# Kernel tuning notes

Hardware: AMD Instinct MI355X
Metric: run time of the kernel (lower is better)

## Reference

```python
import jax, jax.numpy as jnp
import numpy as np

B, L, C = 512, 2048, 32  # batch, seq_len, num_labels


def setup_inputs() -> dict:
    key = jax.random.key(0)
    k1, k2, k3 = jax.random.split(key, 3)
    emissions = jax.random.normal(k1, (B, L, C), dtype=jnp.float32)
    tags = jax.random.randint(k2, (B, L), 0, C, dtype=jnp.int32)
    mask = jnp.ones((B, L), dtype=jnp.int32)
    # learned parameter: transitions (num_labels, num_labels)
    transitions = jax.random.normal(k3, (C, C), dtype=jnp.float32)
    return {"emissions": emissions, "transitions": transitions, "tags": tags, "mask": mask}


def _crf_nll(emissions, transitions, tags, mask):
    Bn, Ln, Cn = emissions.shape
    maskf = mask.astype(emissions.dtype)

    # ---- gold-path score (vectorized over the t loop) ----
    # emit[b,t] = emissions[b,t,tags[b,t]] for t in [0, L-2]
    emit = jnp.take_along_axis(emissions[:, : Ln - 1], tags[:, : Ln - 1, None], axis=2)[..., 0]
    # trans[b,t] = transitions[tags[b,t], tags[b,t+1]]
    trans = transitions[tags[:, : Ln - 1], tags[:, 1:]]
    score = jnp.sum(emit * maskf[:, : Ln - 1] + trans * maskf[:, 1:], axis=1)

    msum = jnp.sum(mask, axis=1)
    last_idx = jnp.clip(msum - 1, 0)  # index of last valid tag
    last_tag = jnp.take_along_axis(tags, last_idx[:, None], axis=1)[:, 0]
    le_t = jnp.clip(msum, 1) - 1
    last_emission = emissions[jnp.arange(Bn), le_t, last_tag]
    score = score + last_emission

    # ---- log-partition via forward algorithm (lax.scan over time) ----
    # Faithful to source: alpha_t[b,n,p] = alpha[b,p] + transitions[n,p] + emit[b,n],
    # reduced over p; the source's mask line is an algebraic no-op (a*m + a*(1-m) = a).
    def step(alpha, emit_t):
        # alpha: (B, C) over prev label p; emit_t: (B, C) over next label n
        alpha_new = jax.nn.logsumexp(alpha[:, None, :] + transitions[None, :, :], axis=2) + emit_t
        return alpha_new, None

    alpha0 = emissions[:, 0]                      # (B, C)
    em_rest = jnp.swapaxes(emissions[:, 1:], 0, 1)  # (L-1, B, C)
    alpha, _ = jax.lax.scan(step, alpha0, em_rest)
    log_Z = jax.nn.logsumexp(alpha, axis=1)       # (B,)

    return jnp.mean(log_Z - score)


def reference(emissions, transitions, tags, mask):
    return _crf_nll(emissions, transitions, tags, mask)
```

## Files before the change

kernel.cpp:

```cpp
#include <hip/hip_runtime.h>
#include <stdint.h>

typedef short bf16x8 __attribute__((ext_vector_type(8)));
typedef float f32x16 __attribute__((ext_vector_type(16)));

#define LOG2E 1.44269504088896340736f
#define LN2f  0.69314718055994530942f

constexpr int Bn = 512;
constexpr int Ln = 2048;
constexpr int Cn = 32;
constexpr int NSEG = 16;
constexpr int SEGLEN = 128;
constexpr int WARM = 16;
constexpr int NGRP = 16;

__device__ __forceinline__ uint32_t pack2_bf16(float lo, float hi) {
    uint32_t a = __float_as_uint(lo) + 0x8000u;
    uint32_t b = __float_as_uint(hi) + 0x8000u;
    return __builtin_amdgcn_perm(b, a, 0x07060302u);
}

__global__ __launch_bounds__(64, 1) void crf_scan(
    const float* __restrict__ emis, const float* __restrict__ trans,
    const int* __restrict__ tags, const int* __restrict__ mask,
    float* __restrict__ dDelta, float* __restrict__ dScore, int* __restrict__ dMsum)
{
    __shared__ float Tlds[Cn * Cn];
    const int lane = threadIdx.x;
    const int h    = lane >> 5;
    const int bl   = lane & 31;
    const int g    = blockIdx.x & (NGRP - 1);
    const int s    = blockIdx.x >> 4;
    const int b    = g * 32 + bl;
    const size_t eb = (size_t)b * Ln * Cn;
    const size_t tB = (size_t)b * Ln;

    for (int i = lane; i < Cn * Cn; i += 64) Tlds[i] = trans[i];

    bf16x8 A1, A2;
    {
        float e1[8], e2[8];
        #pragma unroll
        for (int j = 0; j < 8; ++j) {
            int c1 = 4 * h + (j & 3) + 8 * (j >> 2);
            e1[j] = __expf(trans[bl * Cn + c1]);
            e2[j] = __expf(trans[bl * Cn + c1 + 16]);
        }
        union { uint32_t u[4]; bf16x8 v; } ua, ub;
        #pragma unroll
        for (int q = 0; q < 4; ++q) {
            ua.u[q] = pack2_bf16(e1[2*q], e1[2*q+1]);
            ub.u[q] = pack2_bf16(e2[2*q], e2[2*q+1]);
        }
        A1 = ua.v; A2 = ub.v;
    }

    const f32x16 zeroC = {0.f,0.f,0.f,0.f,0.f,0.f,0.f,0.f,0.f,0.f,0.f,0.f,0.f,0.f,0.f,0.f};

    f32x16 Dv;
    bf16x8 B1, B2;
    float offF = 0.f;
    float adj  = 0.f;
    float score = 0.f;
    int   msum = 0;
    int   prevTag = 0;
    float4 buf[8][4];
    int tcur[8], mcur[8];

    const int t0 = (s == 0) ? 0 : s * SEGLEN - WARM;

    auto loadEm = [&](int t, float4 (&dst)[4]) {
        const float4* p = (const float4*)(emis + eb + (size_t)t * Cn + 4 * h);
        dst[0] = p[0]; dst[1] = p[2]; dst[2] = p[4]; dst[3] = p[6];
    };

    auto packB = [&]() {
        union { uint32_t u[4]; bf16x8 v; } p1, p2;
        #pragma unroll
        for (int q = 0; q < 4; ++q) {
            p1.u[q] = pack2_bf16(Dv[2*q],     Dv[2*q + 1]);
            p2.u[q] = pack2_bf16(Dv[8 + 2*q], Dv[8 + 2*q + 1]);
        }
        B1 = p1.v; B2 = p2.v;
    };

    auto initStep = [&](const float4 (&bu)[4]) {
        #pragma unroll
        for (int q = 0; q < 4; ++q) {
            Dv[4*q+0] = __expf(bu[q].x);
            Dv[4*q+1] = __expf(bu[q].y);
            Dv[4*q+2] = __expf(bu[q].z);
            Dv[4*q+3] = __expf(bu[q].w);
        }
        packB();
    };

    auto stepMfma = [&](const float4 (&bu)[4], float a) {
        f32x16 acc = __builtin_amdgcn_mfma_f32_32x32x16_bf16(A1, B1, zeroC, 0, 0, 0);
        acc = __builtin_amdgcn_mfma_f32_32x32x16_bf16(A2, B2, acc, 0, 0, 0);
        #pragma unroll
        for (int q = 0; q < 4; ++q) {
            float x0 = exp2f(fmaf(bu[q].x, LOG2E, a));
            float x1 = exp2f(fmaf(bu[q].y, LOG2E, a));
            float x2 = exp2f(fmaf(bu[q].z, LOG2E, a));
            float x3 = exp2f(fmaf(bu[q].w, LOG2E, a));
            Dv[4*q+0] = acc[4*q+0] * x0;
            Dv[4*q+1] = acc[4*q+1] * x1;
            Dv[4*q+2] = acc[4*q+2] * x2;
            Dv[4*q+3] = acc[4*q+3] * x3;
        }
        packB();
    };

    auto renorm = [&]() {
        float m0 = fmaxf(fmaxf(Dv[0], Dv[1]),  fmaxf(Dv[2],  Dv[3]));
        float m1 = fmaxf(fmaxf(Dv[4], Dv[5]),  fmaxf(Dv[6],  Dv[7]));
        float m2 = fmaxf(fmaxf(Dv[8], Dv[9]),  fmaxf(Dv[10], Dv[11]));
        float m3 = fmaxf(fmaxf(Dv[12],Dv[13]), fmaxf(Dv[14], Dv[15]));
        float m  = fmaxf(fmaxf(m0, m1), fmaxf(m2, m3));
        m = fmaxf(m, __shfl_xor(m, 32, 64));
        int k = (int)((__float_as_uint(m) >> 23) & 0xffu) - 126;
        offF += (float)k * LN2f;
        adj = -(float)k;
    };

    auto sumD = [&]() {
        float t = 0.f;
        #pragma unroll
        for (int r = 0; r < 16; ++r) t += Dv[r];
        t += __shfl_xor(t, 32, 64);
        return t;
    };

    auto loadTagsMask = [&](int t) {
        int4 a0 = *(const int4*)(tags + tB + t);
        int4 a1 = *(const int4*)(tags + tB + t + 4);
        int4 c0 = *(const int4*)(mask + tB + t);
        int4 c1 = *(const int4*)(mask + tB + t + 4);
        tcur[0]=a0.x; tcur[1]=a0.y; tcur[2]=a0.z; tcur[3]=a0.w;
        tcur[4]=a1.x; tcur[5]=a1.y; tcur[6]=a1.z; tcur[7]=a1.w;
        mcur[0]=c0.x; mcur[1]=c0.y; mcur[2]=c0.z; mcur[3]=c0.w;
        mcur[4]=c1.x; mcur[5]=c1.y; mcur[6]=c1.z; mcur[7]=c1.w;
    };

    auto realBlock = [&](int tb) {
        int tn = min(tb + 8, Ln - 8);
        int4 a0 = *(const int4*)(tags + tB + tn);
        int4 a1 = *(const int4*)(tags + tB + tn + 4);
        int4 c0 = *(const int4*)(mask + tB + tn);
        int4 c1 = *(const int4*)(mask + tB + tn + 4);
        float gv[8];
        #pragma unroll
        for (int u = 0; u < 8; ++u)
            gv[u] = emis[eb + (size_t)(tb + u) * Cn + tcur[u]];
        #pragma unroll
        for (int u = 0; u < 8; ++u) {
            stepMfma(buf[u], (u == 0) ? adj : 0.f);
            loadEm(min(tb + u + 8, Ln - 1), buf[u]);
            float fm = (float)mcur[u];
            msum += mcur[u];
            score += fm * Tlds[(prevTag << 5) + tcur[u]];
            if (tb + u < Ln - 1) score += fm * gv[u];
            prevTag = tcur[u];
        }
        adj = 0.f;
        tcur[0]=a0.x; tcur[1]=a0.y; tcur[2]=a0.z; tcur[3]=a0.w;
        tcur[4]=a1.x; tcur[5]=a1.y; tcur[6]=a1.z; tcur[7]=a1.w;
        mcur[0]=c0.x; mcur[1]=c0.y; mcur[2]=c0.z; mcur[3]=c0.w;
        mcur[4]=c1.x; mcur[5]=c1.y; mcur[6]=c1.z; mcur[7]=c1.w;
    };

    #pragma unroll
    for (int u = 0; u < 8; ++u) loadEm(t0 + u, buf[u]);

    if (s == 0) {
        loadTagsMask(0);
        initStep(buf[0]);
        loadEm(8, buf[0]);
        float g0 = emis[eb + tcur[0]];
        score += (float)mcur[0] * g0;
        msum += mcur[0];
        prevTag = tcur[0];
        float gv[8];
        #pragma unroll
        for (int u = 1; u < 8; ++u) gv[u] = emis[eb + (size_t)u * Cn + tcur[u]];
        #pragma unroll
        for (int u = 1; u < 8; ++u) {
            stepMfma(buf[u], 0.f);
            loadEm(u + 8, buf[u]);
            float fm = (float)mcur[u];
            msum += mcur[u];
            score += fm * Tlds[(prevTag << 5) + tcur[u]];
            score += fm * gv[u];
            prevTag = tcur[u];
        }
        loadTagsMask(8);
        renorm();
        #pragma unroll 1
        for (int blk = 0; blk < 15; ++blk) {
            realBlock(8 + 8 * blk);
            if (blk < 14) renorm();
        }
    } else {
        initStep(buf[0]);
        loadEm(t0 + 8, buf[0]);
        #pragma unroll
        for (int u = 1; u < 8; ++u) {
            stepMfma(buf[u], 0.f);
            loadEm(t0 + 8 + u, buf[u]);
        }
        renorm();
        prevTag = tags[tB + s * SEGLEN - 1];
        loadTagsMask(s * SEGLEN);
        #pragma unroll
        for (int u = 0; u < 8; ++u) {
            stepMfma(buf[u], (u == 0) ? adj : 0.f);
            loadEm(min(t0 + u + 16, Ln - 1), buf[u]);
        }
        adj = 0.f;
        float S = sumD();
        adj = -__log2f(S);
        offF = 0.f;
        #pragma unroll 1
        for (int blk = 0; blk < 16; ++blk) {
            realBlock(s * SEGLEN + 8 * blk);
            if (blk < 15) renorm();
        }
    }

    float Sf = sumD();
    float delta = offF + __logf(Sf);
    if (lane < 32) {
        dDelta[s * Bn + b] = delta;
        dScore[s * Bn + b] = score;
        dMsum [s * Bn + b] = msum;
    }
}

__global__ void crf_final(const float* __restrict__ dDelta, const float* __restrict__ dScore,
                          const int* __restrict__ dMsum, const int* __restrict__ tags,
                          const float* __restrict__ emis, float* __restrict__ out)
{
    __shared__ float red[8];
    int b = threadIdx.x;
    float lz = 0.f, sc = 0.f; int ms = 0;
    #pragma unroll
    for (int s2 = 0; s2 < NSEG; ++s2) {
        lz += dDelta[s2 * Bn + b];
        sc += dScore[s2 * Bn + b];
        ms += dMsum [s2 * Bn + b];
    }
    int last_idx = max(ms - 1, 0);
    int le_t     = max(ms, 1) - 1;
    int lt = tags[(size_t)b * Ln + last_idx];
    float le = emis[((size_t)b * Ln + le_t) * Cn + lt];
    float val = lz - (sc + le);
    #pragma unroll
    for (int o = 32; o > 0; o >>= 1) val += __shfl_down(val, o, 64);
    if ((b & 63) == 0) red[b >> 6] = val;
    __syncthreads();
    if (b == 0) {
        float t = 0.f;
        #pragma unroll
        for (int w = 0; w < 8; ++w) t += red[w];
        out[0] = t * (1.0f / (float)Bn);
    }
}

extern "C" void kernel_launch(void* const* d_in, const int* in_sizes, int n_in,
                              void* d_out, int out_size, void* d_ws, size_t ws_size,
                              hipStream_t stream)
{
    const float* emis  = (const float*)d_in[0];
    const float* trans = (const float*)d_in[1];
    const int*   tags  = (const int*)d_in[2];
    const int*   mask  = (const int*)d_in[3];
    float* wsf = (float*)d_ws;
    float* dDelta = wsf;
    float* dScore = wsf + NSEG * Bn;
    int*   dMsum  = (int*)(wsf + 2 * NSEG * Bn);
    crf_scan<<<NGRP * NSEG, 64, 0, stream>>>(emis, trans, tags, mask, dDelta, dScore, dMsum);
    crf_final<<<1, Bn, 0, stream>>>(dDelta, dScore, dMsum, tags, emis, (float*)d_out);
}
```

Baseline: 219.3 us.

## Split gold-path scoring into separate kernel and double scan segments

The forward-scan kernel drops its gold-path score, tag and mask work, which moves to a new crf_score kernel with one 256-thread block per batch row. The scan now runs 32 segments of 64 steps instead of 16 of 128, doubling the number of blocks to 512 single-wave blocks. The aim is a shorter serial dependency chain per block and less per-step work on the critical scan path. In exchange, the fixed 16-step warm-up becomes a larger share of each segment, emissions are read more times, and an extra kernel launch is added.

After: 232.9 us. 1.06x slower.

```diff
diff --git a/kernel.cpp b/kernel.cpp
--- a/kernel.cpp
+++ b/kernel.cpp
@@ -10,8 +10,8 @@
 constexpr int Bn = 512;
 constexpr int Ln = 2048;
 constexpr int Cn = 32;
-constexpr int NSEG = 16;
-constexpr int SEGLEN = 128;
+constexpr int NSEG = 32;
+constexpr int SEGLEN = 64;
 constexpr int WARM = 16;
 constexpr int NGRP = 16;
 
@@ -23,10 +23,8 @@
 
 __global__ __launch_bounds__(64, 1) void crf_scan(
     const float* __restrict__ emis, const float* __restrict__ trans,
-    const int* __restrict__ tags, const int* __restrict__ mask,
-    float* __restrict__ dDelta, float* __restrict__ dScore, int* __restrict__ dMsum)
-{
-    __shared__ float Tlds[Cn * Cn];
+    float* __restrict__ dDelta)
+{
     const int lane = threadIdx.x;
     const int h    = lane >> 5;
     const int bl   = lane & 31;
@@ -34,9 +32,6 @@
     const int s    = blockIdx.x >> 4;
     const int b    = g * 32 + bl;
     const size_t eb = (size_t)b * Ln * Cn;
-    const size_t tB = (size_t)b * Ln;
-
-    for (int i = lane; i < Cn * Cn; i += 64) Tlds[i] = trans[i];
 
     bf16x8 A1, A2;
     {
@@ -62,11 +57,7 @@
     bf16x8 B1, B2;
     float offF = 0.f;
     float adj  = 0.f;
-    float score = 0.f;
-    int   msum = 0;
-    int   prevTag = 0;
     float4 buf[8][4];
-    int tcur[8], mcur[8];
 
     const int t0 = (s == 0) ? 0 : s * SEGLEN - WARM;
 
@@ -133,129 +124,111 @@
         return t;
     };
 
-    auto loadTagsMask = [&](int t) {
-        int4 a0 = *(const int4*)(tags + tB + t);
-        int4 a1 = *(const int4*)(tags + tB + t + 4);
-        int4 c0 = *(const int4*)(mask + tB + t);
-        int4 c1 = *(const int4*)(mask + tB + t + 4);
-        tcur[0]=a0.x; tcur[1]=a0.y; tcur[2]=a0.z; tcur[3]=a0.w;
-        tcur[4]=a1.x; tcur[5]=a1.y; tcur[6]=a1.z; tcur[7]=a1.w;
-        mcur[0]=c0.x; mcur[1]=c0.y; mcur[2]=c0.z; mcur[3]=c0.w;
-        mcur[4]=c1.x; mcur[5]=c1.y; mcur[6]=c1.z; mcur[7]=c1.w;
-    };
-
-    auto realBlock = [&](int tb) {
-        int tn = min(tb + 8, Ln - 8);
-        int4 a0 = *(const int4*)(tags + tB + tn);
-        int4 a1 = *(const int4*)(tags + tB + tn + 4);
-        int4 c0 = *(const int4*)(mask + tB + tn);
-        int4 c1 = *(const int4*)(mask + tB + tn + 4);
-        float gv[8];
-        #pragma unroll
-        for (int u = 0; u < 8; ++u)
-            gv[u] = emis[eb + (size_t)(tb + u) * Cn + tcur[u]];
+    #pragma unroll
+    for (int u = 0; u < 8; ++u) loadEm(t0 + u, buf[u]);
+
+    initStep(buf[0]);
+    loadEm(t0 + 8, buf[0]);
+    #pragma unroll
+    for (int u = 1; u < 8; ++u) {
+        stepMfma(buf[u], 0.f);
+        loadEm(t0 + 8 + u, buf[u]);
+    }
+    renorm();
+
+    int nblk, tb;
+    if (s == 0) {
+        nblk = 7;
+        tb = 8;
+    } else {
         #pragma unroll
         for (int u = 0; u < 8; ++u) {
             stepMfma(buf[u], (u == 0) ? adj : 0.f);
-            loadEm(min(tb + u + 8, Ln - 1), buf[u]);
-            float fm = (float)mcur[u];
-            msum += mcur[u];
-            score += fm * Tlds[(prevTag << 5) + tcur[u]];
-            if (tb + u < Ln - 1) score += fm * gv[u];
-            prevTag = tcur[u];
-        }
-        adj = 0.f;
-        tcur[0]=a0.x; tcur[1]=a0.y; tcur[2]=a0.z; tcur[3]=a0.w;
-        tcur[4]=a1.x; tcur[5]=a1.y; tcur[6]=a1.z; tcur[7]=a1.w;
-        mcur[0]=c0.x; mcur[1]=c0.y; mcur[2]=c0.z; mcur[3]=c0.w;
-        mcur[4]=c1.x; mcur[5]=c1.y; mcur[6]=c1.z; mcur[7]=c1.w;
-    };
-
-    #pragma unroll
-    for (int u = 0; u < 8; ++u) loadEm(t0 + u, buf[u]);
-
-    if (s == 0) {
-        loadTagsMask(0);
-        initStep(buf[0]);
-        loadEm(8, buf[0]);
-        float g0 = emis[eb + tcur[0]];
-        score += (float)mcur[0] * g0;
-        msum += mcur[0];
-        prevTag = tcur[0];
-        float gv[8];
-        #pragma unroll
-        for (int u = 1; u < 8; ++u) gv[u] = emis[eb + (size_t)u * Cn + tcur[u]];
-        #pragma unroll
-        for (int u = 1; u < 8; ++u) {
-            stepMfma(buf[u], 0.f);
-            loadEm(u + 8, buf[u]);
-            float fm = (float)mcur[u];
-            msum += mcur[u];
-            score += fm * Tlds[(prevTag << 5) + tcur[u]];
-            score += fm * gv[u];
-            prevTag = tcur[u];
-        }
-        loadTagsMask(8);
-        renorm();
-        #pragma unroll 1
-        for (int blk = 0; blk < 15; ++blk) {
-            realBlock(8 + 8 * blk);
-            if (blk < 14) renorm();
-        }
-    } else {
-        initStep(buf[0]);
-        loadEm(t0 + 8, buf[0]);
-        #pragma unroll
-        for (int u = 1; u < 8; ++u) {
-            stepMfma(buf[u], 0.f);
-            loadEm(t0 + 8 + u, buf[u]);
-        }
-        renorm();
-        prevTag = tags[tB + s * SEGLEN - 1];
-        loadTagsMask(s * SEGLEN);
-        #pragma unroll
-        for (int u = 0; u < 8; ++u) {
-            stepMfma(buf[u], (u == 0) ? adj : 0.f);
-            loadEm(min(t0 + u + 16, Ln - 1), buf[u]);
+            loadEm(t0 + 16 + u, buf[u]);
         }
         adj = 0.f;
         float S = sumD();
         adj = -__log2f(S);
         offF = 0.f;
-        #pragma unroll 1
-        for (int blk = 0; blk < 16; ++blk) {
-            realBlock(s * SEGLEN + 8 * blk);
-            if (blk < 15) renorm();
-        }
-    }
-
-    float Sf = sumD();
-    float delta = offF + __logf(Sf);
-    if (lane < 32) {
-        dDelta[s * Bn + b] = delta;
-        dScore[s * Bn + b] = score;
-        dMsum [s * Bn + b] = msum;
-    }
-}
-
-__global__ void crf_final(const float* __restrict__ dDelta, const float* __restrict__ dScore,
-                          const int* __restrict__ dMsum, const int* __restrict__ tags,
-                          const float* __restrict__ emis, float* __restrict__ out)
+        nblk = 8;
+        tb = s * SEGLEN;
+    }
+
+    #pragma unroll 1
+    for (int blk = 0; blk < nblk; ++blk) {
+        #pragma unroll
+        for (int u = 0; u < 8; ++u) {
+            stepMfma(buf[u], (u == 0) ? adj : 0.f);
+            loadEm(min(tb + u + 8, Ln - 1), buf[u]);
+        }
+        adj = 0.f;
+        if (blk < nblk - 1) renorm();
+        tb += 8;
+    }
+
+    float delta = offF + __logf(sumD());
+    if (lane < 32) dDelta[s * Bn + b] = delta;
+}
+
+__global__ __launch_bounds__(256) void crf_score(
+    const float* __restrict__ emis, const float* __restrict__ trans,
+    const int* __restrict__ tags, const int* __restrict__ mask,
+    float* __restrict__ dScore)
+{
+    __shared__ float Tl[Cn * Cn];
+    __shared__ float sred[4];
+    __shared__ int   mred[4];
+    const int b   = blockIdx.x;
+    const int tid = threadIdx.x;
+    for (int i = tid; i < Cn * Cn; i += 256) Tl[i] = trans[i];
+    __syncthreads();
+
+    const size_t tB = (size_t)b * Ln;
+    const size_t eB = (size_t)b * Ln * Cn;
+    float sc = 0.f;
+    int   ms = 0;
+    #pragma unroll
+    for (int k = 0; k < Ln / 256; ++k) {
+        int t  = tid + k * 256;
+        int tg = tags[tB + t];
+        int mk = mask[tB + t];
+        ms += mk;
+        if (t < Ln - 1) {
+            int tg1 = tags[tB + t + 1];
+            int mk1 = mask[tB + t + 1];
+            sc += (float)mk  * emis[eB + (size_t)t * Cn + tg];
+            sc += (float)mk1 * Tl[(tg << 5) + tg1];
+        }
+    }
+    #pragma unroll
+    for (int o = 32; o > 0; o >>= 1) {
+        sc += __shfl_down(sc, o, 64);
+        ms += __shfl_down(ms, o, 64);
+    }
+    if ((tid & 63) == 0) { sred[tid >> 6] = sc; mred[tid >> 6] = ms; }
+    __syncthreads();
+    if (tid == 0) {
+        float S = 0.f; int M = 0;
+        #pragma unroll
+        for (int w = 0; w < 4; ++w) { S += sred[w]; M += mred[w]; }
+        int last_idx = max(M - 1, 0);
+        int le_t     = max(M, 1) - 1;
+        int lt = tags[tB + last_idx];
+        float le = emis[(tB + le_t) * Cn + lt];
+        dScore[b] = S + le;
+    }
+}
+
+__global__ void crf_final(const float* __restrict__ dDelta,
+                          const float* __restrict__ dScore,
+                          float* __restrict__ out)
 {
     __shared__ float red[8];
     int b = threadIdx.x;
-    float lz = 0.f, sc = 0.f; int ms = 0;
-    #pragma unroll
-    for (int s2 = 0; s2 < NSEG; ++s2) {
-        lz += dDelta[s2 * Bn + b];
-        sc += dScore[s2 * Bn + b];
-        ms += dMsum [s2 * Bn + b];
-    }
-    int last_idx = max(ms - 1, 0);
-    int le_t     = max(ms, 1) - 1;
-    int lt = tags[(size_t)b * Ln + last_idx];
-    float le = emis[((size_t)b * Ln + le_t) * Cn + lt];
-    float val = lz - (sc + le);
+    float lz = 0.f;
+    #pragma unroll
+    for (int s2 = 0; s2 < NSEG; ++s2) lz += dDelta[s2 * Bn + b];
+    float val = lz - dScore[b];
     #pragma unroll
     for (int o = 32; o > 0; o >>= 1) val += __shfl_down(val, o, 64);
     if ((b & 63) == 0) red[b >> 6] = val;
@@ -279,7 +252,7 @@
     float* wsf = (float*)d_ws;
     float* dDelta = wsf;
     float* dScore = wsf + NSEG * Bn;
-    int*   dMsum  = (int*)(wsf + 2 * NSEG * Bn);
-    crf_scan<<<NGRP * NSEG, 64, 0, stream>>>(emis, trans, tags, mask, dDelta, dScore, dMsum);
-    crf_final<<<1, Bn, 0, stream>>>(dDelta, dScore, dMsum, tags, emis, (float*)d_out);
-}
+    crf_scan <<<NGRP * NSEG, 64, 0, stream>>>(emis, trans, dDelta);
+    crf_score<<<Bn, 256, 0, stream>>>(emis, trans, tags, mask, dScore);
+    crf_final<<<1, Bn, 0, stream>>>(dDelta, dScore, (float*)d_out);
+}
```
